# Optimization experiments

Measured on AMD Instinct MI355X. Metric: run time of the kernel, lower is better.

## Reference

```python
import jax, jax.numpy as jnp
import numpy as np

N, E, F_IN = 50000, 1_600_000, 256
HID, HEADS, NCLS = 8, 8, 16  # conv1: 8 heads x 8 dims (concat=64); conv2: 1 head -> 16 classes


def setup_inputs() -> dict:
    key = jax.random.key(0)
    ks = jax.random.split(key, 11)
    x = jax.random.normal(ks[0], (N, F_IN), dtype=jnp.float32)
    edge_index = jax.random.randint(ks[1], (2, E), 0, N, dtype=jnp.int32)
    s1 = 1.0 / np.sqrt(F_IN)
    W1 = jax.random.normal(ks[2], (F_IN, HEADS * HID), jnp.float32) * s1
    a_src1 = jax.random.normal(ks[3], (HEADS, HID), jnp.float32) * 0.1
    a_dst1 = jax.random.normal(ks[4], (HEADS, HID), jnp.float32) * 0.1
    b1 = jnp.zeros((HEADS * HID,), jnp.float32)
    s2 = 1.0 / np.sqrt(HEADS * HID)
    W2 = jax.random.normal(ks[5], (HEADS * HID, NCLS), jnp.float32) * s2
    a_src2 = jax.random.normal(ks[6], (1, NCLS), jnp.float32) * 0.1
    a_dst2 = jax.random.normal(ks[7], (1, NCLS), jnp.float32) * 0.1
    b2 = jnp.zeros((NCLS,), jnp.float32)
    return {"x": x, "edge_index": edge_index, "W1": W1, "a_src1": a_src1,
            "a_dst1": a_dst1, "b1": b1, "W2": W2, "a_src2": a_src2,
            "a_dst2": a_dst2, "b2": b2}


def _gat_conv(x, W, a_src, a_dst, bias, src, dst, n, heads, ch, concat):
    # per-head linear transform: [n, heads, ch]
    h = (x @ W).reshape(n, heads, ch)
    # additive attention logits per node, per head
    al_s = jnp.einsum('nhc,hc->nh', h, a_src)
    al_d = jnp.einsum('nhc,hc->nh', h, a_dst)
    e = jax.nn.leaky_relu(al_s[src] + al_d[dst], 0.2)  # [E_tot, heads]
    # segment softmax grouped by destination node (self-loops guarantee non-empty segments)
    m = jax.ops.segment_max(e, dst, num_segments=n)
    ex = jnp.exp(e - m[dst])
    den = jax.ops.segment_sum(ex, dst, num_segments=n)
    alpha = ex / den[dst]  # [E_tot, heads]
    # scatter-aggregate weighted neighbor features
    out = jax.ops.segment_sum(h[src] * alpha[:, :, None], dst, num_segments=n)
    out = out.reshape(n, heads * ch) if concat else out.mean(axis=1)
    return out + bias


def reference(x, edge_index, W1, a_src1, a_dst1, b1, W2, a_src2, a_dst2, b2):
    # add self-loops (PyG GATConv default)
    loops = jnp.arange(N, dtype=edge_index.dtype)
    src = jnp.concatenate([edge_index[0], loops])
    dst = jnp.concatenate([edge_index[1], loops])
    h = _gat_conv(x, W1, a_src1, a_dst1, b1, src, dst, N, HEADS, HID, True)
    h = jax.nn.elu(h)
    out = _gat_conv(h, W2, a_src2, a_dst2, b2, src, dst, N, 1, NCLS, False)
    return jax.nn.log_softmax(out, axis=1)
```

## Files before the change

### kernel.cpp

```cpp
#include <hip/hip_runtime.h>
#include <hip/hip_fp16.h>

#define NN   50000
#define FIN  256
#define C1   64
#define NH   8
#define NHID 8
#define NC   16
#define NE   1600000
#define NTOT (NE + NN)

#define CH   256
#define EPC  ((NTOT + CH - 1) / CH)
#define NCB  196

typedef _Float16 half8 __attribute__((ext_vector_type(8)));
typedef float f32x4 __attribute__((ext_vector_type(4)));

#define OFF_H1H   0
#define OFF_H2    0
#define OFF_ALS2  800000
#define OFF_ALD2  850000
#define OFF_G1    3200000
#define OFF_ALS1  6400000
#define OFF_ALD1  6800000
#define OFF_HM    7200000
#define OFF_BASEK 7251000
#define OFF_BBASE 7302000
#define OFF_OFFS  7302400
#define OFF_SRC   7352500

__global__ __launch_bounds__(256) void k_gemm1(const float* __restrict__ x,
                                               const float* __restrict__ W1,
                                               const float* __restrict__ as1,
                                               const float* __restrict__ ad1,
                                               __half* __restrict__ h1h,
                                               float* __restrict__ als,
                                               float* __restrict__ ald) {
    __shared__ _Float16 wsT[64][264];
    __shared__ _Float16 xs[64][40];
    const int tid = threadIdx.x;
    const int r0 = blockIdx.x * 64;

    for (int i = tid; i < FIN * C1; i += 256) {
        int k = i >> 6, c = i & 63;
        wsT[c][k] = (_Float16)W1[i];
    }

    const int lane = tid & 63;
    const int wv   = tid >> 6;
    const int colb = lane & 15;
    const int rgrp = lane >> 4;
    f32x4 acc[4] = {};

    const int srow = tid >> 2;
    const int sq   = tid & 3;
    for (int k0 = 0; k0 < FIN; k0 += 32) {
        __syncthreads();
        {
            int grow = r0 + srow;
            float4 v0 = make_float4(0.f,0.f,0.f,0.f), v1 = v0;
            if (grow < NN) {
                const float4* xp = (const float4*)(&x[(size_t)grow * FIN + k0 + sq * 8]);
                v0 = xp[0]; v1 = xp[1];
            }
            half8 hv;
            hv[0]=(_Float16)v0.x; hv[1]=(_Float16)v0.y; hv[2]=(_Float16)v0.z; hv[3]=(_Float16)v0.w;
            hv[4]=(_Float16)v1.x; hv[5]=(_Float16)v1.y; hv[6]=(_Float16)v1.z; hv[7]=(_Float16)v1.w;
            *(half8*)(&xs[srow][sq * 8]) = hv;
        }
        __syncthreads();
        half8 a = *(half8*)(&xs[wv * 16 + colb][rgrp * 8]);
        #pragma unroll
        for (int ct = 0; ct < 4; ++ct) {
            half8 b = *(half8*)(&wsT[ct * 16 + colb][k0 + rgrp * 8]);
            acc[ct] = __builtin_amdgcn_mfma_f32_16x16x32_f16(a, b, acc[ct], 0, 0, 0);
        }
    }

    float a_s[4], a_d[4];
    #pragma unroll
    for (int ct = 0; ct < 4; ++ct) { a_s[ct] = as1[ct * 16 + colb]; a_d[ct] = ad1[ct * 16 + colb]; }
    #pragma unroll
    for (int j = 0; j < 4; ++j) {
        int row = r0 + wv * 16 + rgrp * 4 + j;
        bool rv = row < NN;
        #pragma unroll
        for (int ct = 0; ct < 4; ++ct) {
            if (rv) h1h[(size_t)row * C1 + ct * 16 + colb] = __float2half(acc[ct][j]);
            float p = acc[ct][j] * a_s[ct];
            p += __shfl_xor(p, 1); p += __shfl_xor(p, 2); p += __shfl_xor(p, 4);
            float q = acc[ct][j] * a_d[ct];
            q += __shfl_xor(q, 1); q += __shfl_xor(q, 2); q += __shfl_xor(q, 4);
            if (rv && (lane & 7) == 0) {
                int head = ct * 2 + (colb >> 3);
                als[row * NH + head] = p;
                ald[row * NH + head] = q;
            }
        }
    }
}

__global__ __launch_bounds__(256) void k_rh(const int* __restrict__ ei,
                                            int* __restrict__ H) {
    __shared__ int lh[NCB];
    int k = blockIdx.x;
    for (int i = threadIdx.x; i < NCB; i += 256) lh[i] = 0;
    __syncthreads();
    int e0 = k * EPC, e1 = min(e0 + EPC, NTOT);
    for (int e = e0 + threadIdx.x; e < e1; e += 256) {
        int d = (e < NE) ? ei[NE + e] : (e - NE);
        atomicAdd(&lh[d >> 8], 1);
    }
    __syncthreads();
    for (int i = threadIdx.x; i < NCB; i += 256) H[k * NCB + i] = lh[i];
}

__global__ __launch_bounds__(256) void k_rsA(const int* __restrict__ H,
                                             int* __restrict__ basek,
                                             int* __restrict__ btot) {
    __shared__ int sc[CH];
    int b = blockIdx.x, t = threadIdx.x;
    int v = H[t * NCB + b];
    sc[t] = v;
    __syncthreads();
    for (int s = 1; s < CH; s <<= 1) {
        int u = (t >= s) ? sc[t - s] : 0;
        __syncthreads();
        sc[t] += u;
        __syncthreads();
    }
    basek[b * CH + t] = sc[t] - v;
    if (t == CH - 1) btot[b] = sc[t];
}

__global__ __launch_bounds__(64) void k_rsB(int* __restrict__ btot,
                                            int* __restrict__ bbase,
                                            int* __restrict__ offs) {
    if (threadIdx.x == 0) {
        int run = 0;
        for (int b = 0; b < NCB; ++b) {
            bbase[b] = run;
            run += btot[b];
        }
        bbase[NCB] = run;
        offs[NN] = NTOT;
    }
}

__global__ __launch_bounds__(256) void k_rscatter(const int* __restrict__ ei,
                                                  const int* __restrict__ basek,
                                                  const int* __restrict__ bbase,
                                                  int* __restrict__ stage) {
    __shared__ int lcur[NCB];
    int k = blockIdx.x;
    for (int i = threadIdx.x; i < NCB; i += 256)
        lcur[i] = bbase[i] + basek[i * CH + k];
    __syncthreads();
    int e0 = k * EPC, e1 = min(e0 + EPC, NTOT);
    for (int e = e0 + threadIdx.x; e < e1; e += 256) {
        int s, d;
        if (e < NE) { s = ei[e]; d = ei[NE + e]; }
        else        { s = e - NE; d = s; }
        int pos = atomicAdd(&lcur[d >> 8], 1);
        stage[pos] = (s << 8) | (d & 255);
    }
}

__global__ __launch_bounds__(256) void k_fsort(const int* __restrict__ stage,
                                               const int* __restrict__ bbase,
                                               int* __restrict__ offs,
                                               int* __restrict__ ssrc) {
    __shared__ int lc[256];
    __shared__ int ls[256];
    __shared__ int lcur[256];
    int b = blockIdx.x, t = threadIdx.x;
    int base = bbase[b];
    int n = bbase[b + 1] - base;
    lc[t] = 0;
    __syncthreads();
    const int* sp = &stage[base];
    for (int i = t; i < n; i += 256) atomicAdd(&lc[sp[i] & 255], 1);
    __syncthreads();
    int v = lc[t];
    ls[t] = v;
    __syncthreads();
    for (int s = 1; s < 256; s <<= 1) {
        int u = (t >= s) ? ls[t - s] : 0;
        __syncthreads();
        ls[t] += u;
        __syncthreads();
    }
    int excl = ls[t] - v;
    int d = b * 256 + t;
    if (d < NN) offs[d] = base + excl;
    lcur[t] = base + excl;
    __syncthreads();
    for (int i = t; i < n; i += 256) {
        int u = sp[i];
        int pos = atomicAdd(&lcur[u & 255], 1);
        ssrc[pos] = u >> 8;
    }
}

__global__ __launch_bounds__(256) void k_agg1(const int* __restrict__ offs,
                                              const int* __restrict__ src,
                                              const __half* __restrict__ h1h,
                                              const float* __restrict__ als,
                                              const float* __restrict__ ald,
                                              const float* __restrict__ b1,
                                              float* __restrict__ g1) {
    int d = blockIdx.x * 4 + (threadIdx.x >> 6);
    if (d >= NN) return;
    const int l = threadIdx.x & 63;
    const int sub = l >> 3, hh = l & 7;
    const int hf = l >> 5, cp = l & 31;
    const int hp = cp >> 2;
    int beg = offs[d], end = offs[d + 1];
    float aldv = ald[d * NH + hh];
    float accx = 0.f, accy = 0.f, den = 0.f;
    for (int r = beg; r < end; r += 16) {
        int e0 = r + sub, e1 = r + 8 + sub;
        bool v0 = e0 < end, v1 = e1 < end;
        int s0 = src[v0 ? e0 : end - 1];
        int s1 = src[v1 ? e1 : end - 1];
        float lg0 = als[s0 * NH + hh] + aldv;
        float lg1 = als[s1 * NH + hh] + aldv;
        lg0 = lg0 > 0.f ? lg0 : 0.2f * lg0;
        lg1 = lg1 > 0.f ? lg1 : 0.2f * lg1;
        float w0 = v0 ? __expf(lg0) : 0.f;
        float w1 = v1 ? __expf(lg1) : 0.f;
        #pragma unroll
        for (int i = 0; i < 4; ++i) {
            int srcl = (2 * i + hf) * 8;
            int sv0   = __shfl(s0, srcl);
            float wv0 = __shfl(w0, srcl + hp);
            int sv1   = __shfl(s1, srcl);
            float wv1 = __shfl(w1, srcl + hp);
            float2 h0 = __half22float2(*(const __half2*)(&h1h[(size_t)sv0 * C1 + 2 * cp]));
            float2 h1v = __half22float2(*(const __half2*)(&h1h[(size_t)sv1 * C1 + 2 * cp]));
            accx += wv0 * h0.x + wv1 * h1v.x;
            accy += wv0 * h0.y + wv1 * h1v.y;
            den  += wv0 + wv1;
        }
    }
    accx += __shfl_xor(accx, 32);
    accy += __shfl_xor(accy, 32);
    den  += __shfl_xor(den, 32);
    float o0 = accx / den + b1[2 * cp];
    float o1 = accy / den + b1[2 * cp + 1];
    o0 = o0 > 0.f ? o0 : (__expf(o0) - 1.f);
    o1 = o1 > 0.f ? o1 : (__expf(o1) - 1.f);
    if (hf == 0)
        *(float2*)(&g1[(size_t)d * C1 + 2 * cp]) = make_float2(o0, o1);
}

__global__ __launch_bounds__(256) void k_gemm2(const float* __restrict__ g1,
                                               const float* __restrict__ W2,
                                               const float* __restrict__ as2,
                                               const float* __restrict__ ad2,
                                               float* __restrict__ h2,
                                               float* __restrict__ als2,
                                               float* __restrict__ ald2) {
    __shared__ float w2s[C1][NC];
    __shared__ float hact[16][C1 + 4];
    int tid = threadIdx.x;
    for (int i = tid; i < C1 * NC; i += 256) w2s[i >> 4][i & 15] = W2[i];
    int ln = tid >> 4, j = tid & 15;
    int n = blockIdx.x * 16 + ln;
    if (n < NN) {
        float4 v = *(const float4*)(&g1[(size_t)n * C1 + j * 4]);
        *(float4*)(&hact[ln][j * 4]) = v;
    }
    __syncthreads();
    if (n < NN) {
        float sum = 0.f;
        #pragma unroll
        for (int c = 0; c < C1; ++c) sum += hact[ln][c] * w2s[c][j];
        h2[(size_t)n * NC + j] = sum;
        float ps = sum * as2[j], pd = sum * ad2[j];
        #pragma unroll
        for (int w = 1; w < 16; w <<= 1) {
            ps += __shfl_xor(ps, w);
            pd += __shfl_xor(pd, w);
        }
        if (j == 0) { als2[n] = ps; ald2[n] = pd; }
    }
}

__global__ __launch_bounds__(256) void k_agg2(const int* __restrict__ offs,
                                              const int* __restrict__ src,
                                              const float* __restrict__ h2,
                                              const float* __restrict__ als2,
                                              const float* __restrict__ ald2,
                                              const float* __restrict__ b2,
                                              float* __restrict__ out) {
    int d = blockIdx.x * 16 + (threadIdx.x >> 4);
    if (d >= NN) return;
    int c = threadIdx.x & 15;
    int beg = offs[d], end = offs[d + 1];
    float aldv = ald2[d];
    float acc = 0.f, den = 0.f;
    for (int r = beg; r < end; r += 4) {
        int e1 = r + 1, e2 = r + 2, e3 = r + 3;
        bool v1 = e1 < end, v2 = e2 < end, v3 = e3 < end;
        int s0 = src[r];
        int s1 = src[v1 ? e1 : end - 1];
        int s2 = src[v2 ? e2 : end - 1];
        int s3 = src[v3 ? e3 : end - 1];
        float l0 = als2[s0] + aldv;
        float l1 = als2[s1] + aldv;
        float l2 = als2[s2] + aldv;
        float l3 = als2[s3] + aldv;
        l0 = l0 > 0.f ? l0 : 0.2f * l0;
        l1 = l1 > 0.f ? l1 : 0.2f * l1;
        l2 = l2 > 0.f ? l2 : 0.2f * l2;
        l3 = l3 > 0.f ? l3 : 0.2f * l3;
        float w0 = __expf(l0);
        float w1 = v1 ? __expf(l1) : 0.f;
        float w2 = v2 ? __expf(l2) : 0.f;
        float w3 = v3 ? __expf(l3) : 0.f;
        float f0 = h2[(size_t)s0 * NC + c];
        float f1 = h2[(size_t)s1 * NC + c];
        float f2 = h2[(size_t)s2 * NC + c];
        float f3 = h2[(size_t)s3 * NC + c];
        acc += w0 * f0 + w1 * f1 + w2 * f2 + w3 * f3;
        den += w0 + w1 + w2 + w3;
    }
    float o = acc / den + b2[c];
    float m = o;
    #pragma unroll
    for (int w = 1; w < 16; w <<= 1) m = fmaxf(m, __shfl_xor(m, w));
    float ex = __expf(o - m);
    float sm = ex;
    #pragma unroll
    for (int w = 1; w < 16; w <<= 1) sm += __shfl_xor(sm, w);
    out[(size_t)d * NC + c] = o - m - __logf(sm);
}

extern "C" void kernel_launch(void* const* d_in, const int* in_sizes, int n_in,
                              void* d_out, int out_size, void* d_ws, size_t ws_size,
                              hipStream_t stream) {
    const float* x   = (const float*)d_in[0];
    const int*   ei  = (const int*)  d_in[1];
    const float* W1  = (const float*)d_in[2];
    const float* as1 = (const float*)d_in[3];
    const float* ad1 = (const float*)d_in[4];
    const float* b1  = (const float*)d_in[5];
    const float* W2  = (const float*)d_in[6];
    const float* as2 = (const float*)d_in[7];
    const float* ad2 = (const float*)d_in[8];
    const float* b2  = (const float*)d_in[9];
    float* ws  = (float*)d_ws;
    float* out = (float*)d_out;

    __half* h1h = (__half*)(ws + OFF_H1H);
    float* g1   = ws + OFF_G1;
    float* als1 = ws + OFF_ALS1;
    float* ald1 = ws + OFF_ALD1;
    float* h2   = ws + OFF_H2;
    float* als2 = ws + OFF_ALS2;
    float* ald2 = ws + OFF_ALD2;
    int* H      = (int*)(ws + OFF_HM);
    int* basek  = (int*)(ws + OFF_BASEK);
    int* bbase  = (int*)(ws + OFF_BBASE);
    int* offs   = (int*)(ws + OFF_OFFS);
    int* ssrc   = (int*)(ws + OFF_SRC);
    int* stage  = (int*)(ws + OFF_G1);

    k_gemm1   <<<(NN + 63) / 64, 256, 0, stream>>>(x, W1, as1, ad1, h1h, als1, ald1);
    k_rh      <<<CH,             256, 0, stream>>>(ei, H);
    k_rsA     <<<NCB,            256, 0, stream>>>(H, basek, bbase + NCB + 2 );
    k_rsB     <<<1,               64, 0, stream>>>(bbase + NCB + 2, bbase, offs);
    k_rscatter<<<CH,             256, 0, stream>>>(ei, basek, bbase, stage);
    k_fsort   <<<NCB,            256, 0, stream>>>(stage, bbase, offs, ssrc);
    k_agg1    <<<(NN + 3) / 4,   256, 0, stream>>>(offs, ssrc, h1h, als1, ald1, b1, g1);
    k_gemm2   <<<(NN + 15) / 16, 256, 0, stream>>>(g1, W2, as2, ad2, h2, als2, ald2);
    k_agg2    <<<(NN + 15) / 16, 256, 0, stream>>>(offs, ssrc, h2, als2, ald2, b2, out);
}
```

Baseline: 148.8 us.

## Fuse layer-2 GEMM into agg1 epilogue, merge histogram into GEMM1, fp16 h2

Fuses the histogram kernel into the first GEMM launch as extra blocks. It computes the 64x16 second-layer projection and its attention logits directly in the agg1 epilogue, so the fp32 g1 intermediate is never written or read back. h2 is stored in fp16 to halve gather traffic in agg2. agg1 lanes now load 4 halves at a time. This adds some LDS work per block and some extra rounding error from the fp16 h2.

```diff
diff --git a/kernel.cpp b/kernel.cpp
--- a/kernel.cpp
+++ b/kernel.cpp
@@ -5,7 +5,6 @@
 #define FIN  256
 #define C1   64
 #define NH   8
-#define NHID 8
 #define NC   16
 #define NE   1600000
 #define NTOT (NE + NN)
@@ -13,15 +12,17 @@
 #define CH   256
 #define EPC  ((NTOT + CH - 1) / CH)
 #define NCB  196
+#define GB1  ((NN + 63) / 64)
 
 typedef _Float16 half8 __attribute__((ext_vector_type(8)));
+typedef _Float16 half4 __attribute__((ext_vector_type(4)));
 typedef float f32x4 __attribute__((ext_vector_type(4)));
 
 #define OFF_H1H   0
-#define OFF_H2    0
-#define OFF_ALS2  800000
-#define OFF_ALD2  850000
-#define OFF_G1    3200000
+#define OFF_H2H   1600000
+#define OFF_ALS2  2000000
+#define OFF_ALD2  2050000
+#define OFF_STAGE 3200000
 #define OFF_ALS1  6400000
 #define OFF_ALD1  6800000
 #define OFF_HM    7200000
@@ -30,21 +31,46 @@
 #define OFF_OFFS  7302400
 #define OFF_SRC   7352500
 
-__global__ __launch_bounds__(256) void k_gemm1(const float* __restrict__ x,
-                                               const float* __restrict__ W1,
-                                               const float* __restrict__ as1,
-                                               const float* __restrict__ ad1,
-                                               __half* __restrict__ h1h,
-                                               float* __restrict__ als,
-                                               float* __restrict__ ald) {
+__global__ __launch_bounds__(256) void k_g1rh(const float* __restrict__ x,
+                                              const float* __restrict__ W1,
+                                              const float* __restrict__ as1,
+                                              const float* __restrict__ ad1,
+                                              __half* __restrict__ h1h,
+                                              float* __restrict__ als,
+                                              float* __restrict__ ald,
+                                              const int* __restrict__ ei,
+                                              int* __restrict__ H) {
     __shared__ _Float16 wsT[64][264];
     __shared__ _Float16 xs[64][40];
+    __shared__ int lh[NCB];
     const int tid = threadIdx.x;
+
+    if (blockIdx.x >= GB1) {
+        int k = blockIdx.x - GB1;
+        for (int i = tid; i < NCB; i += 256) lh[i] = 0;
+        __syncthreads();
+        int e0 = k * EPC, e1 = min(e0 + EPC, NTOT);
+        for (int e = e0 + tid; e < e1; e += 256) {
+            int d = (e < NE) ? ei[NE + e] : (e - NE);
+            atomicAdd(&lh[d >> 8], 1);
+        }
+        __syncthreads();
+        for (int i = tid; i < NCB; i += 256) H[k * NCB + i] = lh[i];
+        return;
+    }
+
     const int r0 = blockIdx.x * 64;
-
-    for (int i = tid; i < FIN * C1; i += 256) {
-        int k = i >> 6, c = i & 63;
-        wsT[c][k] = (_Float16)W1[i];
+    {
+        int c = tid & 63, kb = tid >> 6;
+        #pragma unroll
+        for (int j = 0; j < 8; ++j) {
+            int k8 = kb + 4 * j;
+            half8 hv;
+            #pragma unroll
+            for (int u = 0; u < 8; ++u)
+                hv[u] = (_Float16)W1[(size_t)(k8 * 8 + u) * C1 + c];
+            *(half8*)(&wsT[c][k8 * 8]) = hv;
+        }
     }
 
     const int lane = tid & 63;
@@ -52,7 +78,6 @@
     const int colb = lane & 15;
     const int rgrp = lane >> 4;
     f32x4 acc[4] = {};
-
     const int srow = tid >> 2;
     const int sq   = tid & 3;
     for (int k0 = 0; k0 < FIN; k0 += 32) {
@@ -101,21 +126,6 @@
     }
 }
 
-__global__ __launch_bounds__(256) void k_rh(const int* __restrict__ ei,
-                                            int* __restrict__ H) {
-    __shared__ int lh[NCB];
-    int k = blockIdx.x;
-    for (int i = threadIdx.x; i < NCB; i += 256) lh[i] = 0;
-    __syncthreads();
-    int e0 = k * EPC, e1 = min(e0 + EPC, NTOT);
-    for (int e = e0 + threadIdx.x; e < e1; e += 256) {
-        int d = (e < NE) ? ei[NE + e] : (e - NE);
-        atomicAdd(&lh[d >> 8], 1);
-    }
-    __syncthreads();
-    for (int i = threadIdx.x; i < NCB; i += 256) H[k * NCB + i] = lh[i];
-}
-
 __global__ __launch_bounds__(256) void k_rsA(const int* __restrict__ H,
                                              int* __restrict__ basek,
                                              int* __restrict__ btot) {
@@ -209,88 +219,90 @@
                                               const float* __restrict__ als,
                                               const float* __restrict__ ald,
                                               const float* __restrict__ b1,
-                                              float* __restrict__ g1) {
-    int d = blockIdx.x * 4 + (threadIdx.x >> 6);
+                                              const float* __restrict__ W2,
+                                              const float* __restrict__ as2,
+                                              const float* __restrict__ ad2,
+                                              __half* __restrict__ h2h,
+                                              float* __restrict__ als2,
+                                              float* __restrict__ ald2) {
+    __shared__ float lds_w2[C1][17];
+    __shared__ float lds_g[4][C1];
+    int tid = threadIdx.x;
+    #pragma unroll
+    for (int i = tid; i < C1 * NC; i += 256) lds_w2[i >> 4][i & 15] = W2[i];
+    __syncthreads();
+
+    int wv = tid >> 6;
+    int d = blockIdx.x * 4 + wv;
     if (d >= NN) return;
-    const int l = threadIdx.x & 63;
-    const int sub = l >> 3, hh = l & 7;
-    const int hf = l >> 5, cp = l & 31;
-    const int hp = cp >> 2;
+    const int l  = tid & 63;
+    const int q  = l >> 4, lc = l & 15;
+    const int hg = lc >> 1;
+    const int sub = l >> 3, hw = l & 7;
+    const int lane_a = (q << 3) | hg;
+    const int lane_b = lane_a + 32;
     int beg = offs[d], end = offs[d + 1];
-    float aldv = ald[d * NH + hh];
-    float accx = 0.f, accy = 0.f, den = 0.f;
+    float aldv = ald[d * NH + hw];
+    f32x4 acc = {0.f, 0.f, 0.f, 0.f};
+    float den = 0.f;
+
     for (int r = beg; r < end; r += 16) {
-        int e0 = r + sub, e1 = r + 8 + sub;
+        int e0 = r + sub, e1 = e0 + 8;
         bool v0 = e0 < end, v1 = e1 < end;
         int s0 = src[v0 ? e0 : end - 1];
         int s1 = src[v1 ? e1 : end - 1];
-        float lg0 = als[s0 * NH + hh] + aldv;
-        float lg1 = als[s1 * NH + hh] + aldv;
+        float lg0 = als[s0 * NH + hw] + aldv;
+        float lg1 = als[s1 * NH + hw] + aldv;
         lg0 = lg0 > 0.f ? lg0 : 0.2f * lg0;
         lg1 = lg1 > 0.f ? lg1 : 0.2f * lg1;
         float w0 = v0 ? __expf(lg0) : 0.f;
         float w1 = v1 ? __expf(lg1) : 0.f;
         #pragma unroll
         for (int i = 0; i < 4; ++i) {
-            int srcl = (2 * i + hf) * 8;
-            int sv0   = __shfl(s0, srcl);
-            float wv0 = __shfl(w0, srcl + hp);
-            int sv1   = __shfl(s1, srcl);
-            float wv1 = __shfl(w1, srcl + hp);
-            float2 h0 = __half22float2(*(const __half2*)(&h1h[(size_t)sv0 * C1 + 2 * cp]));
-            float2 h1v = __half22float2(*(const __half2*)(&h1h[(size_t)sv1 * C1 + 2 * cp]));
-            accx += wv0 * h0.x + wv1 * h1v.x;
-            accy += wv0 * h0.y + wv1 * h1v.y;
-            den  += wv0 + wv1;
-        }
-    }
-    accx += __shfl_xor(accx, 32);
-    accy += __shfl_xor(accy, 32);
-    den  += __shfl_xor(den, 32);
-    float o0 = accx / den + b1[2 * cp];
-    float o1 = accy / den + b1[2 * cp + 1];
-    o0 = o0 > 0.f ? o0 : (__expf(o0) - 1.f);
-    o1 = o1 > 0.f ? o1 : (__expf(o1) - 1.f);
-    if (hf == 0)
-        *(float2*)(&g1[(size_t)d * C1 + 2 * cp]) = make_float2(o0, o1);
-}
-
-__global__ __launch_bounds__(256) void k_gemm2(const float* __restrict__ g1,
-                                               const float* __restrict__ W2,
-                                               const float* __restrict__ as2,
-                                               const float* __restrict__ ad2,
-                                               float* __restrict__ h2,
-                                               float* __restrict__ als2,
-                                               float* __restrict__ ald2) {
-    __shared__ float w2s[C1][NC];
-    __shared__ float hact[16][C1 + 4];
-    int tid = threadIdx.x;
-    for (int i = tid; i < C1 * NC; i += 256) w2s[i >> 4][i & 15] = W2[i];
-    int ln = tid >> 4, j = tid & 15;
-    int n = blockIdx.x * 16 + ln;
-    if (n < NN) {
-        float4 v = *(const float4*)(&g1[(size_t)n * C1 + j * 4]);
-        *(float4*)(&hact[ln][j * 4]) = v;
-    }
-    __syncthreads();
-    if (n < NN) {
-        float sum = 0.f;
-        #pragma unroll
-        for (int c = 0; c < C1; ++c) sum += hact[ln][c] * w2s[c][j];
-        h2[(size_t)n * NC + j] = sum;
-        float ps = sum * as2[j], pd = sum * ad2[j];
-        #pragma unroll
-        for (int w = 1; w < 16; w <<= 1) {
-            ps += __shfl_xor(ps, w);
-            pd += __shfl_xor(pd, w);
-        }
-        if (j == 0) { als2[n] = ps; ald2[n] = pd; }
-    }
+            int srcl = (i & 1) ? lane_b : lane_a;
+            int sv   = __shfl((i < 2) ? s0 : s1, srcl);
+            float wvv= __shfl((i < 2) ? w0 : w1, srcl);
+            half4 hv = *(const half4*)(&h1h[(size_t)sv * C1 + 4 * lc]);
+            acc[0] += wvv * (float)hv[0];
+            acc[1] += wvv * (float)hv[1];
+            acc[2] += wvv * (float)hv[2];
+            acc[3] += wvv * (float)hv[3];
+            den += wvv;
+        }
+    }
+    #pragma unroll
+    for (int k = 0; k < 4; ++k) {
+        acc[k] += __shfl_xor(acc[k], 16);
+        acc[k] += __shfl_xor(acc[k], 32);
+    }
+    den += __shfl_xor(den, 16);
+    den += __shfl_xor(den, 32);
+
+    float g[4];
+    #pragma unroll
+    for (int k = 0; k < 4; ++k) {
+        float o = acc[k] / den + b1[4 * lc + k];
+        g[k] = o > 0.f ? o : (__expf(o) - 1.f);
+    }
+    if (q == 0) *(float4*)(&lds_g[wv][4 * lc]) = make_float4(g[0], g[1], g[2], g[3]);
+    float h2p = 0.f;
+    #pragma unroll
+    for (int m = 0; m < 16; ++m)
+        h2p += lds_g[wv][q * 16 + m] * lds_w2[q * 16 + m][lc];
+    h2p += __shfl_xor(h2p, 16);
+    h2p += __shfl_xor(h2p, 32);
+    if (l < 16) h2h[(size_t)d * NC + lc] = __float2half(h2p);
+    float ps = h2p * as2[lc], pd = h2p * ad2[lc];
+    ps += __shfl_xor(ps, 1); ps += __shfl_xor(ps, 2);
+    ps += __shfl_xor(ps, 4); ps += __shfl_xor(ps, 8);
+    pd += __shfl_xor(pd, 1); pd += __shfl_xor(pd, 2);
+    pd += __shfl_xor(pd, 4); pd += __shfl_xor(pd, 8);
+    if (l == 0) { als2[d] = ps; ald2[d] = pd; }
 }
 
 __global__ __launch_bounds__(256) void k_agg2(const int* __restrict__ offs,
                                               const int* __restrict__ src,
-                                              const float* __restrict__ h2,
+                                              const __half* __restrict__ h2h,
                                               const float* __restrict__ als2,
                                               const float* __restrict__ ald2,
                                               const float* __restrict__ b2,
@@ -320,10 +332,10 @@
         float w1 = v1 ? __expf(l1) : 0.f;
         float w2 = v2 ? __expf(l2) : 0.f;
         float w3 = v3 ? __expf(l3) : 0.f;
-        float f0 = h2[(size_t)s0 * NC + c];
-        float f1 = h2[(size_t)s1 * NC + c];
-        float f2 = h2[(size_t)s2 * NC + c];
-        float f3 = h2[(size_t)s3 * NC + c];
+        float f0 = __half2float(h2h[(size_t)s0 * NC + c]);
+        float f1 = __half2float(h2h[(size_t)s1 * NC + c]);
+        float f2 = __half2float(h2h[(size_t)s2 * NC + c]);
+        float f3 = __half2float(h2h[(size_t)s3 * NC + c]);
         acc += w0 * f0 + w1 * f1 + w2 * f2 + w3 * f3;
         den += w0 + w1 + w2 + w3;
     }
@@ -355,10 +367,9 @@
     float* out = (float*)d_out;
 
     __half* h1h = (__half*)(ws + OFF_H1H);
-    float* g1   = ws + OFF_G1;
+    __half* h2h = (__half*)(ws + OFF_H2H);
     float* als1 = ws + OFF_ALS1;
     float* ald1 = ws + OFF_ALD1;
-    float* h2   = ws + OFF_H2;
     float* als2 = ws + OFF_ALS2;
     float* ald2 = ws + OFF_ALD2;
     int* H      = (int*)(ws + OFF_HM);
@@ -366,15 +377,14 @@
     int* bbase  = (int*)(ws + OFF_BBASE);
     int* offs   = (int*)(ws + OFF_OFFS);
     int* ssrc   = (int*)(ws + OFF_SRC);
-    int* stage  = (int*)(ws + OFF_G1);
-
-    k_gemm1   <<<(NN + 63) / 64, 256, 0, stream>>>(x, W1, as1, ad1, h1h, als1, ald1);
-    k_rh      <<<CH,             256, 0, stream>>>(ei, H);
+    int* stage  = (int*)(ws + OFF_STAGE);
+
+    k_g1rh    <<<GB1 + CH,       256, 0, stream>>>(x, W1, as1, ad1, h1h, als1, ald1, ei, H);
     k_rsA     <<<NCB,            256, 0, stream>>>(H, basek, bbase + NCB + 2 );
     k_rsB     <<<1,               64, 0, stream>>>(bbase + NCB + 2, bbase, offs);
     k_rscatter<<<CH,             256, 0, stream>>>(ei, basek, bbase, stage);
     k_fsort   <<<NCB,            256, 0, stream>>>(stage, bbase, offs, ssrc);
-    k_agg1    <<<(NN + 3) / 4,   256, 0, stream>>>(offs, ssrc, h1h, als1, ald1, b1, g1);
-    k_gemm2   <<<(NN + 15) / 16, 256, 0, stream>>>(g1, W2, as2, ad2, h2, als2, ald2);
-    k_agg2    <<<(NN + 15) / 16, 256, 0, stream>>>(offs, ssrc, h2, als2, ald2, b2, out);
-}
+    k_agg1    <<<(NN + 3) / 4,   256, 0, stream>>>(offs, ssrc, h1h, als1, ald1, b1,
+                                                   W2, as2, ad2, h2h, als2, ald2);
+    k_agg2    <<<(NN + 15) / 16, 256, 0, stream>>>(offs, ssrc, h2h, als2, ald2, b2, out);
+}
```

New measurement: 142.7 us. -4.1%, faster.
